# Performance work log

Hardware: AMD Instinct MI355X
Metric: run time of the kernel (lower is better)

The kernel has to match this reference:

```python
import jax, jax.numpy as jnp
import numpy as np

DMODEL, DK, DV, NHEAD = 512, 64, 64, 8
MASK_VALUE = -10000000.0


def setup_inputs() -> dict:
    key = jax.random.key(0)
    ks = jax.random.split(key, 12)
    b, slen = 8, 1024
    inputs = jax.random.normal(ks[0], (b, slen, DMODEL), dtype=jnp.float32)
    mask = (jax.random.uniform(ks[1], (b, slen, slen)) < 0.1).astype(jnp.float32)
    s = 1.0 / np.sqrt(DMODEL)
    wq = jax.random.uniform(ks[2], (DK * NHEAD, DMODEL), minval=-s, maxval=s, dtype=jnp.float32)
    bq = jnp.zeros((DK * NHEAD,), jnp.float32)
    wk = jax.random.uniform(ks[3], (DK * NHEAD, DMODEL), minval=-s, maxval=s, dtype=jnp.float32)
    bk = jnp.zeros((DK * NHEAD,), jnp.float32)
    wv = jax.random.uniform(ks[4], (DV * NHEAD, DMODEL), minval=-s, maxval=s, dtype=jnp.float32)
    bv = jnp.zeros((DV * NHEAD,), jnp.float32)
    wo = jax.random.uniform(ks[5], (DMODEL, NHEAD * DV), minval=-s, maxval=s, dtype=jnp.float32)
    bo = jnp.zeros((DMODEL,), jnp.float32)
    return {"inputs": inputs, "mask": mask, "wq": wq, "bq": bq, "wk": wk,
            "bk": bk, "wv": wv, "bv": bv, "wo": wo, "bo": bo}


def mask_logits(target, mask, mask_value=MASK_VALUE):
    return target * (1.0 - mask) + mask * mask_value


def reference(inputs, mask, wq, bq, wk, bk, wv, bv, wo, bo):
    b, slen, _ = inputs.shape
    scale = np.power(DK, 0.5).astype(np.float32)
    # projections -> [b, slen, nhead, d] -> [b, nhead, slen, d]
    q = (inputs @ wq.T + bq).reshape(b, slen, NHEAD, DK).transpose(0, 2, 1, 3)
    k = (inputs @ wk.T + bk).reshape(b, slen, NHEAD, DK).transpose(0, 2, 1, 3)
    v = (inputs @ wv.T + bv).reshape(b, slen, NHEAD, DV).transpose(0, 2, 1, 3)
    # scores [b, h, s, s]
    score = jnp.einsum("bhqd,bhkd->bhqk", q, k) / scale
    m = mask[:, None, :, :]  # broadcast over heads (original repeats mask per head)
    score = mask_logits(score, m)
    attn = jax.nn.softmax(score, axis=-1)
    attn = mask_logits(attn, m, 0.0)  # second zeroing mask pass
    # dropout is identity in eval mode
    out = jnp.einsum("bhqk,bhkd->bhqd", attn, v)  # [b, h, s, dv]
    out = out.transpose(0, 2, 1, 3).reshape(b, slen, NHEAD * DV)
    return out @ wo.T + bo
```

## Files before the change

### kernel.cpp

```cpp
#include <hip/hip_runtime.h>
#include <cstdint>
#include <cstddef>

#define NHEAD 8
#define SLEN 1024

typedef __bf16 bf16x8 __attribute__((ext_vector_type(8)));
typedef float f32x4 __attribute__((ext_vector_type(4)));

__device__ inline unsigned short f2bf(float f) {
    union { float f; unsigned int u; } v; v.f = f;
    unsigned int u = v.u;
    unsigned int rounded = u + 0x7fffu + ((u >> 16) & 1u);
    return (unsigned short)(rounded >> 16);
}

__device__ inline unsigned int pack2(float a, float b) {
    return (unsigned int)f2bf(a) | ((unsigned int)f2bf(b) << 16);
}

__device__ inline unsigned int cvtpk2(float lo, float hi) {
    unsigned int r;
    asm("v_cvt_pk_bf16_f32 %0, %1, %2" : "=v"(r) : "v"(lo), "v"(hi));
    return r;
}

__device__ inline void gll16(const unsigned short* g, unsigned short* l) {
    __builtin_amdgcn_global_load_lds(
        (const __attribute__((address_space(1))) unsigned int*)g,
        (__attribute__((address_space(3))) unsigned int*)l,
        16, 0, 0);
}

__device__ inline uint4 cvt8(const float* __restrict__ p) {
    float4 a = *reinterpret_cast<const float4*>(p);
    float4 b = *reinterpret_cast<const float4*>(p + 4);
    uint4 r;
    r.x = pack2(a.x, a.y);
    r.y = pack2(a.z, a.w);
    r.z = pack2(b.x, b.y);
    r.w = pack2(b.z, b.w);
    return r;
}

__global__ __launch_bounds__(256) void prep(
    const float* __restrict__ X,
    const float* __restrict__ wq, const float* __restrict__ wk,
    const float* __restrict__ wv, const float* __restrict__ wo,
    const float* __restrict__ mask,
    unsigned short* __restrict__ Xb, unsigned short* __restrict__ Wc,
    unsigned long long* __restrict__ bits)
{
    int y = blockIdx.y;
    if (y == 5) {
        int wid = (blockIdx.x * 256 + threadIdx.x) >> 6;
        int lane = threadIdx.x & 63;
        for (int s = 0; s < 16; s++) {
            size_t seg = (size_t)wid * 16 + s;
            float mv = mask[seg * 64 + lane];
            unsigned long long bb = __ballot(mv != 0.0f);
            if (lane == 0) bits[seg] = bb;
        }
        return;
    }
    const float* src;
    unsigned short* dst;
    int n;
    if (y == 0) { src = X;  dst = Xb; n = 8192 * 512; }
    else {
        src = (y == 1) ? wq : (y == 2) ? wk : (y == 3) ? wv : wo;
        dst = Wc + (size_t)(y - 1) * 262144;
        n = 262144;
    }
    int i = (blockIdx.x * 256 + threadIdx.x) * 8;
    if (i + 8 <= n) {
        uint4 v = cvt8(src + i);
        *reinterpret_cast<uint4*>(dst + i) = v;
    }
}

__global__ __launch_bounds__(256) void qkv_gemm(
    const unsigned short* __restrict__ Xb,
    const unsigned short* __restrict__ Wc,
    const float* __restrict__ bq, const float* __restrict__ bk,
    const float* __restrict__ bv,
    unsigned short* __restrict__ Qb, unsigned short* __restrict__ Kb,
    unsigned short* __restrict__ Vtb)
{
    __shared__ unsigned short As[128 * 136];
    unsigned short* Bs = As + 128 * 64;
    const int tid = threadIdx.x;
    const int w = tid >> 6, lane = tid & 63, l15 = lane & 15, quad = lane >> 4;
    const int wm = w & 1, wn = w >> 1;
    const int r0 = blockIdx.x * 128;
    const int ytile = blockIdx.y;
    const int c0 = ytile * 128;
    const unsigned short* Wsel = Wc + (size_t)(ytile >> 2) * 262144;
    const int cw = c0 & 511;

    f32x4 zero = {0.0f, 0.0f, 0.0f, 0.0f};
    f32x4 acc[4][4];
    for (int i = 0; i < 4; i++)
        for (int j = 0; j < 4; j++) acc[i][j] = zero;

    const int lrow = lane >> 3;
    const int lcol = (lane & 7) * 8;

    for (int k0 = 0; k0 < 512; k0 += 64) {
        const unsigned short* gA = Xb + (size_t)(r0 + w * 32 + lrow) * 512 + k0 + lcol;
        const unsigned short* gB = Wsel + (size_t)(cw + w * 32 + lrow) * 512 + k0 + lcol;
        unsigned short* lA = As + (w * 32) * 64;
        unsigned short* lB = Bs + (w * 32) * 64;
        #pragma unroll
        for (int i = 0; i < 4; i++) {
            gll16(gA + i * 8 * 512, lA + i * 8 * 64);
            gll16(gB + i * 8 * 512, lB + i * 8 * 64);
        }
        __syncthreads();
        for (int kc = 0; kc < 64; kc += 32) {
            bf16x8 af[4], bfr[4];
            for (int mi = 0; mi < 4; mi++)
                af[mi] = *reinterpret_cast<const bf16x8*>(As + (wm * 64 + mi * 16 + l15) * 64 + kc + quad * 8);
            for (int ni = 0; ni < 4; ni++)
                bfr[ni] = *reinterpret_cast<const bf16x8*>(Bs + (wn * 64 + ni * 16 + l15) * 64 + kc + quad * 8);
            for (int mi = 0; mi < 4; mi++)
                for (int ni = 0; ni < 4; ni++)
                    acc[mi][ni] = __builtin_amdgcn_mfma_f32_16x16x32_bf16(af[mi], bfr[ni], acc[mi][ni], 0, 0, 0);
        }
        __syncthreads();
    }

    const int bb = r0 >> 10;
    const int s0 = r0 & 1023;

    if (ytile < 8) {
        const bool isQ = (ytile < 4);
        const float* bias = isQ ? bq : bk;
        unsigned short* dst = isQ ? Qb : Kb;
        const float scale = isQ ? 0.125f : 1.0f;
        const int h0 = cw >> 6;
        for (int mi = 0; mi < 4; mi++) {
            for (int ni = 0; ni < 4; ni++) {
                int col = wn * 64 + ni * 16 + l15;
                float bsv = bias[cw + col];
                for (int r = 0; r < 4; r++) {
                    int s_local = wm * 64 + mi * 16 + quad * 4 + r;
                    As[s_local * 136 + col] = f2bf((acc[mi][ni][r] + bsv) * scale);
                }
            }
        }
        __syncthreads();
        for (int p = 0; p < 2; p++) {
            size_t base = (((size_t)(bb * NHEAD + h0 + p)) << 10) + s0;
            for (int i = 0; i < 4; i++) {
                int flat = i * 256 + tid;
                int row = flat >> 3;
                int ch = flat & 7;
                uint4 vv = *reinterpret_cast<const uint4*>(As + row * 136 + p * 64 + ch * 8);
                *reinterpret_cast<uint4*>(dst + (base + row) * 64 + ch * 8) = vv;
            }
        }
    } else {
        const int h_base = (c0 - 1024) >> 6;
        for (int p = 0; p < 2; p++) {
            __syncthreads();
            if (wn == p) {
                for (int mi = 0; mi < 4; mi++) {
                    for (int ni = 0; ni < 4; ni++) {
                        int d_local = ni * 16 + l15;
                        float bias = bv[(h_base + p) * 64 + d_local];
                        for (int r = 0; r < 4; r++) {
                            int s_local = wm * 64 + mi * 16 + quad * 4 + r;
                            As[d_local * 136 + s_local] = f2bf(acc[mi][ni][r] + bias);
                        }
                    }
                }
            }
            __syncthreads();
            int sidx = (tid & 15) * 8;
            int drow = tid >> 4;
            for (int dg = 0; dg < 4; dg++) {
                int d = dg * 16 + drow;
                size_t dst = ((size_t)(bb * NHEAD + h_base + p) * 64 + d) * 1024 + s0;
                uint4 vv = *reinterpret_cast<const uint4*>(As + d * 136 + sidx);
                *reinterpret_cast<uint4*>(Vtb + dst + sidx) = vv;
            }
        }
    }
}

__global__ __launch_bounds__(256, 4) void attn_kernel(
    const unsigned short* __restrict__ Qb,
    const unsigned short* __restrict__ Kb,
    const unsigned short* __restrict__ Vtb,
    const unsigned long long* __restrict__ Mbits,
    unsigned short* __restrict__ Ob)
{
    __shared__ unsigned short KVs[3 * 64 * 72];

    const int tid = threadIdx.x;
    const int w = tid >> 6, lane = tid & 63, l15 = lane & 15, quad = lane >> 4;
    const int flat = blockIdx.x;
    const int bh = flat & 63;
    const int qt = flat >> 6;
    const int b = bh >> 3, h = bh & 7;
    const int q = qt * 64 + w * 16 + l15;
    const unsigned short* Qg = Qb + (size_t)bh * SLEN * 64;
    const unsigned short* Kg = Kb + (size_t)bh * SLEN * 64;
    const unsigned short* Vg = Vtb + (size_t)bh * 64 * SLEN;
    const unsigned long long* mrow = Mbits + ((size_t)b * SLEN + q) * 16;
    unsigned short* Ks = KVs;
    unsigned short* Vs = KVs + 4608;
    unsigned short* Prow = KVs + 9216 + (size_t)(w * 16 + l15) * 72;

    bf16x8 bq0 = *reinterpret_cast<const bf16x8*>(Qg + (size_t)q * 64 + quad * 8);
    bf16x8 bq1 = *reinterpret_cast<const bf16x8*>(Qg + (size_t)q * 64 + 32 + quad * 8);

    f32x4 zero = {0.0f, 0.0f, 0.0f, 0.0f};
    f32x4 Oacc[4];
    for (int nd = 0; nd < 4; nd++) Oacc[nd] = zero;
    float lsum0 = 0.0f, lsum1 = 0.0f;

    const int srow = tid >> 3;
    const int sc8 = (tid & 7) * 8;

    uint4 kr0, kr1, vr0, vr1;
    {
        const unsigned short* kp = Kg + (size_t)srow * 64 + sc8;
        kr0 = *reinterpret_cast<const uint4*>(kp);
        kr1 = *reinterpret_cast<const uint4*>(kp + 32 * 64);
        const unsigned short* vp = Vg + (size_t)srow * SLEN + sc8;
        vr0 = *reinterpret_cast<const uint4*>(vp);
        vr1 = *reinterpret_cast<const uint4*>(vp + (size_t)32 * SLEN);
    }

    for (int kt = 0; kt < 16; kt++) {
        *reinterpret_cast<uint4*>(Ks + srow * 72 + sc8) = kr0;
        *reinterpret_cast<uint4*>(Ks + (srow + 32) * 72 + sc8) = kr1;
        *reinterpret_cast<uint4*>(Vs + srow * 72 + sc8) = vr0;
        *reinterpret_cast<uint4*>(Vs + (srow + 32) * 72 + sc8) = vr1;
        __syncthreads();

        if (kt < 15) {
            int k0n = (kt + 1) * 64;
            const unsigned short* kp = Kg + (size_t)(k0n + srow) * 64 + sc8;
            kr0 = *reinterpret_cast<const uint4*>(kp);
            kr1 = *reinterpret_cast<const uint4*>(kp + 32 * 64);
            const unsigned short* vp = Vg + (size_t)srow * SLEN + k0n + sc8;
            vr0 = *reinterpret_cast<const uint4*>(vp);
            vr1 = *reinterpret_cast<const uint4*>(vp + (size_t)32 * SLEN);
        }

        f32x4 st[4];
        for (int ni = 0; ni < 4; ni++) {
            const unsigned short* kp = Ks + (ni * 16 + l15) * 72 + quad * 8;
            bf16x8 ka0 = *reinterpret_cast<const bf16x8*>(kp);
            bf16x8 ka1 = *reinterpret_cast<const bf16x8*>(kp + 32);
            f32x4 z = zero;
            z = __builtin_amdgcn_mfma_f32_16x16x32_bf16(ka0, bq0, z, 0, 0, 0);
            z = __builtin_amdgcn_mfma_f32_16x16x32_bf16(ka1, bq1, z, 0, 0, 0);
            st[ni] = z;
        }

        unsigned long long mv = mrow[kt] >> (quad * 4);
        unsigned int lo = (unsigned int)mv, hi = (unsigned int)(mv >> 32);
        for (int ni = 0; ni < 4; ni++) {
            unsigned int word = (ni & 2) ? hi : lo;
            int sh = (ni & 1) ? 16 : 0;
            float p0 = ((word >> (sh + 0)) & 1u) ? 0.0f : __expf(st[ni][0]);
            float p1 = ((word >> (sh + 1)) & 1u) ? 0.0f : __expf(st[ni][1]);
            float p2 = ((word >> (sh + 2)) & 1u) ? 0.0f : __expf(st[ni][2]);
            float p3 = ((word >> (sh + 3)) & 1u) ? 0.0f : __expf(st[ni][3]);
            lsum0 += (p0 + p1);
            lsum1 += (p2 + p3);
            uint2 pk;
            pk.x = cvtpk2(p0, p1);
            pk.y = cvtpk2(p2, p3);
            *reinterpret_cast<uint2*>(Prow + ni * 16 + quad * 4) = pk;
        }

        bf16x8 pb0 = *reinterpret_cast<const bf16x8*>(Prow + quad * 8);
        bf16x8 pb1 = *reinterpret_cast<const bf16x8*>(Prow + 32 + quad * 8);
        for (int nd = 0; nd < 4; nd++) {
            const unsigned short* vb = Vs + (nd * 16 + l15) * 72 + quad * 8;
            bf16x8 va0 = *reinterpret_cast<const bf16x8*>(vb);
            bf16x8 va1 = *reinterpret_cast<const bf16x8*>(vb + 32);
            Oacc[nd] = __builtin_amdgcn_mfma_f32_16x16x32_bf16(va0, pb0, Oacc[nd], 0, 0, 0);
            Oacc[nd] = __builtin_amdgcn_mfma_f32_16x16x32_bf16(va1, pb1, Oacc[nd], 0, 0, 0);
        }
        __syncthreads();
    }

    float l = lsum0 + lsum1;
    l += __shfl_xor(l, 16);
    l += __shfl_xor(l, 32);
    float inv = (l > 0.0f) ? (1.0f / l) : 0.0f;
    for (int nd = 0; nd < 4; nd++) {
        uint2 o;
        o.x = cvtpk2(Oacc[nd][0] * inv, Oacc[nd][1] * inv);
        o.y = cvtpk2(Oacc[nd][2] * inv, Oacc[nd][3] * inv);
        *reinterpret_cast<uint2*>(Ob + ((size_t)(b * SLEN + q)) * 512 + h * 64 + nd * 16 + quad * 4) = o;
    }
}

__global__ __launch_bounds__(256) void out_gemm(
    const unsigned short* __restrict__ Ob,
    const unsigned short* __restrict__ Wob,
    const float* __restrict__ bo,
    float* __restrict__ out)
{
    __shared__ unsigned short As[2 * 128 * 64];
    unsigned short* Bs = As + 128 * 64;
    const int tid = threadIdx.x;
    const int w = tid >> 6, lane = tid & 63, l15 = lane & 15, quad = lane >> 4;
    const int wm = w & 1, wn = w >> 1;
    const int r0 = blockIdx.x * 128;
    const int c0 = blockIdx.y * 128;

    f32x4 zero = {0.0f, 0.0f, 0.0f, 0.0f};
    f32x4 acc[4][4];
    for (int i = 0; i < 4; i++)
        for (int j = 0; j < 4; j++) acc[i][j] = zero;

    const int lrow = lane >> 3;
    const int lcol = (lane & 7) * 8;

    for (int k0 = 0; k0 < 512; k0 += 64) {
        const unsigned short* gA = Ob + (size_t)(r0 + w * 32 + lrow) * 512 + k0 + lcol;
        const unsigned short* gB = Wob + (size_t)(c0 + w * 32 + lrow) * 512 + k0 + lcol;
        unsigned short* lA = As + (w * 32) * 64;
        unsigned short* lB = Bs + (w * 32) * 64;
        #pragma unroll
        for (int i = 0; i < 4; i++) {
            gll16(gA + i * 8 * 512, lA + i * 8 * 64);
            gll16(gB + i * 8 * 512, lB + i * 8 * 64);
        }
        __syncthreads();
        for (int kc = 0; kc < 64; kc += 32) {
            bf16x8 af[4], bfr[4];
            for (int mi = 0; mi < 4; mi++)
                af[mi] = *reinterpret_cast<const bf16x8*>(As + (wm * 64 + mi * 16 + l15) * 64 + kc + quad * 8);
            for (int ni = 0; ni < 4; ni++)
                bfr[ni] = *reinterpret_cast<const bf16x8*>(Bs + (wn * 64 + ni * 16 + l15) * 64 + kc + quad * 8);
            for (int mi = 0; mi < 4; mi++)
                for (int ni = 0; ni < 4; ni++)
                    acc[mi][ni] = __builtin_amdgcn_mfma_f32_16x16x32_bf16(af[mi], bfr[ni], acc[mi][ni], 0, 0, 0);
        }
        __syncthreads();
    }

    for (int mi = 0; mi < 4; mi++) {
        int grow_base = r0 + wm * 64 + mi * 16 + quad * 4;
        for (int ni = 0; ni < 4; ni++) {
            int gcol = c0 + wn * 64 + ni * 16 + l15;
            float bias = bo[gcol];
            for (int r = 0; r < 4; r++) {
                int grow = grow_base + r;
                out[(size_t)grow * 512 + gcol] = acc[mi][ni][r] + bias;
            }
        }
    }
}

extern "C" void kernel_launch(void* const* d_in, const int* in_sizes, int n_in,
                              void* d_out, int out_size, void* d_ws, size_t ws_size,
                              hipStream_t stream) {
    (void)in_sizes; (void)n_in; (void)out_size; (void)ws_size;
    const float* x    = (const float*)d_in[0];
    const float* mask = (const float*)d_in[1];
    const float* wq   = (const float*)d_in[2];
    const float* bq   = (const float*)d_in[3];
    const float* wk   = (const float*)d_in[4];
    const float* bk   = (const float*)d_in[5];
    const float* wv   = (const float*)d_in[6];
    const float* bv   = (const float*)d_in[7];
    const float* wo   = (const float*)d_in[8];
    const float* bo   = (const float*)d_in[9];
    float* out = (float*)d_out;

    char* ws = (char*)d_ws;
    unsigned short* Qb   = (unsigned short*)(ws);
    unsigned short* Kb   = (unsigned short*)(ws + 8388608);
    unsigned short* Vtb  = (unsigned short*)(ws + 16777216);
    unsigned short* XO   = (unsigned short*)(ws + 25165824);
    unsigned short* Wc   = (unsigned short*)(ws + 33554432);
    unsigned long long* Mbits = (unsigned long long*)(ws + 35651584);

    prep<<<dim3(2048, 6), 256, 0, stream>>>(x, wq, wk, wv, wo, mask, XO, Wc, Mbits);
    qkv_gemm<<<dim3(64, 12), 256, 0, stream>>>(XO, Wc, bq, bk, bv, Qb, Kb, Vtb);
    attn_kernel<<<dim3(1024), 256, 0, stream>>>(Qb, Kb, Vtb, Mbits, XO );
    out_gemm<<<dim3(64, 4), 256, 0, stream>>>(XO , Wc + 3 * 262144, bo, out);
}
```

Before: 198.4 us.

## Fold log2e into Q scale for raw exp2, and halve out_gemm row tile

Multiplies the Q projection scale by log2(e) so the attention kernel can use the hardware v_exp_f32 (base-2) instruction directly instead of __expf, which drops a multiply per score. Separately, the output GEMM tile shrinks from 128x128 to 64x128 rows per block, which doubles the grid to 512 blocks to improve occupancy and CU coverage on a small GEMM. The trade-off is less reuse of each weight tile and more total global loads for the weights. Dropping the max subtraction is unchanged from before, so overflow risk is the same.

```diff
diff --git a/kernel.cpp b/kernel.cpp
--- a/kernel.cpp
+++ b/kernel.cpp
@@ -25,7 +25,13 @@
     return r;
 }
 
-__device__ inline void gll16(const unsigned short* g, unsigned short* l) {
+__device__ inline float exp2i(float x) {
+    float r;
+    asm("v_exp_f32 %0, %1" : "=v"(r) : "v"(x));
+    return r;
+}
+
+__device__ inline void gll16(const void* g, void* l) {
     __builtin_amdgcn_global_load_lds(
         (const __attribute__((address_space(1))) unsigned int*)g,
         (__attribute__((address_space(3))) unsigned int*)l,
@@ -113,8 +119,8 @@
         unsigned short* lB = Bs + (w * 32) * 64;
         #pragma unroll
         for (int i = 0; i < 4; i++) {
-            gll16(gA + i * 8 * 512, lA + i * 8 * 64);
-            gll16(gB + i * 8 * 512, lB + i * 8 * 64);
+            gll16(gA + (size_t)i * 8 * 512, lA + i * 8 * 64);
+            gll16(gB + (size_t)i * 8 * 512, lB + i * 8 * 64);
         }
         __syncthreads();
         for (int kc = 0; kc < 64; kc += 32) {
@@ -137,7 +143,7 @@
         const bool isQ = (ytile < 4);
         const float* bias = isQ ? bq : bk;
         unsigned short* dst = isQ ? Qb : Kb;
-        const float scale = isQ ? 0.125f : 1.0f;
+        const float scale = isQ ? 0.18033688f : 1.0f;
         const int h0 = cw >> 6;
         for (int mi = 0; mi < 4; mi++) {
             for (int ni = 0; ni < 4; ni++) {
@@ -267,10 +273,10 @@
         for (int ni = 0; ni < 4; ni++) {
             unsigned int word = (ni & 2) ? hi : lo;
             int sh = (ni & 1) ? 16 : 0;
-            float p0 = ((word >> (sh + 0)) & 1u) ? 0.0f : __expf(st[ni][0]);
-            float p1 = ((word >> (sh + 1)) & 1u) ? 0.0f : __expf(st[ni][1]);
-            float p2 = ((word >> (sh + 2)) & 1u) ? 0.0f : __expf(st[ni][2]);
-            float p3 = ((word >> (sh + 3)) & 1u) ? 0.0f : __expf(st[ni][3]);
+            float p0 = ((word >> (sh + 0)) & 1u) ? 0.0f : exp2i(st[ni][0]);
+            float p1 = ((word >> (sh + 1)) & 1u) ? 0.0f : exp2i(st[ni][1]);
+            float p2 = ((word >> (sh + 2)) & 1u) ? 0.0f : exp2i(st[ni][2]);
+            float p3 = ((word >> (sh + 3)) & 1u) ? 0.0f : exp2i(st[ni][3]);
             lsum0 += (p0 + p1);
             lsum1 += (p2 + p3);
             uint2 pk;
@@ -309,50 +315,50 @@
     const float* __restrict__ bo,
     float* __restrict__ out)
 {
-    __shared__ unsigned short As[2 * 128 * 64];
-    unsigned short* Bs = As + 128 * 64;
+    __shared__ unsigned short As[64 * 64 + 128 * 64];
+    unsigned short* Bs = As + 64 * 64;
     const int tid = threadIdx.x;
     const int w = tid >> 6, lane = tid & 63, l15 = lane & 15, quad = lane >> 4;
-    const int wm = w & 1, wn = w >> 1;
-    const int r0 = blockIdx.x * 128;
+    const int r0 = blockIdx.x * 64;
     const int c0 = blockIdx.y * 128;
 
     f32x4 zero = {0.0f, 0.0f, 0.0f, 0.0f};
-    f32x4 acc[4][4];
+    f32x4 acc[4][2];
     for (int i = 0; i < 4; i++)
-        for (int j = 0; j < 4; j++) acc[i][j] = zero;
+        for (int j = 0; j < 2; j++) acc[i][j] = zero;
 
     const int lrow = lane >> 3;
     const int lcol = (lane & 7) * 8;
 
     for (int k0 = 0; k0 < 512; k0 += 64) {
-        const unsigned short* gA = Ob + (size_t)(r0 + w * 32 + lrow) * 512 + k0 + lcol;
+        const unsigned short* gA = Ob + (size_t)(r0 + w * 16 + lrow) * 512 + k0 + lcol;
+        unsigned short* lA = As + (w * 16) * 64;
+        #pragma unroll
+        for (int i = 0; i < 2; i++)
+            gll16(gA + (size_t)i * 8 * 512, lA + i * 8 * 64);
         const unsigned short* gB = Wob + (size_t)(c0 + w * 32 + lrow) * 512 + k0 + lcol;
-        unsigned short* lA = As + (w * 32) * 64;
         unsigned short* lB = Bs + (w * 32) * 64;
         #pragma unroll
-        for (int i = 0; i < 4; i++) {
-            gll16(gA + i * 8 * 512, lA + i * 8 * 64);
-            gll16(gB + i * 8 * 512, lB + i * 8 * 64);
-        }
+        for (int i = 0; i < 4; i++)
+            gll16(gB + (size_t)i * 8 * 512, lB + i * 8 * 64);
         __syncthreads();
         for (int kc = 0; kc < 64; kc += 32) {
-            bf16x8 af[4], bfr[4];
+            bf16x8 af[4], bfr[2];
             for (int mi = 0; mi < 4; mi++)
-                af[mi] = *reinterpret_cast<const bf16x8*>(As + (wm * 64 + mi * 16 + l15) * 64 + kc + quad * 8);
-            for (int ni = 0; ni < 4; ni++)
-                bfr[ni] = *reinterpret_cast<const bf16x8*>(Bs + (wn * 64 + ni * 16 + l15) * 64 + kc + quad * 8);
+                af[mi] = *reinterpret_cast<const bf16x8*>(As + (mi * 16 + l15) * 64 + kc + quad * 8);
+            for (int ni = 0; ni < 2; ni++)
+                bfr[ni] = *reinterpret_cast<const bf16x8*>(Bs + (w * 32 + ni * 16 + l15) * 64 + kc + quad * 8);
             for (int mi = 0; mi < 4; mi++)
-                for (int ni = 0; ni < 4; ni++)
+                for (int ni = 0; ni < 2; ni++)
                     acc[mi][ni] = __builtin_amdgcn_mfma_f32_16x16x32_bf16(af[mi], bfr[ni], acc[mi][ni], 0, 0, 0);
         }
         __syncthreads();
     }
 
     for (int mi = 0; mi < 4; mi++) {
-        int grow_base = r0 + wm * 64 + mi * 16 + quad * 4;
-        for (int ni = 0; ni < 4; ni++) {
-            int gcol = c0 + wn * 64 + ni * 16 + l15;
+        int grow_base = r0 + mi * 16 + quad * 4;
+        for (int ni = 0; ni < 2; ni++) {
+            int gcol = c0 + w * 32 + ni * 16 + l15;
             float bias = bo[gcol];
             for (int r = 0; r < 4; r++) {
                 int grow = grow_base + r;
@@ -389,5 +395,5 @@
     prep<<<dim3(2048, 6), 256, 0, stream>>>(x, wq, wk, wv, wo, mask, XO, Wc, Mbits);
     qkv_gemm<<<dim3(64, 12), 256, 0, stream>>>(XO, Wc, bq, bk, bv, Qb, Kb, Vtb);
     attn_kernel<<<dim3(1024), 256, 0, stream>>>(Qb, Kb, Vtb, Mbits, XO );
-    out_gemm<<<dim3(64, 4), 256, 0, stream>>>(XO , Wc + 3 * 262144, bo, out);
-}
+    out_gemm<<<dim3(128, 4), 256, 0, stream>>>(XO , Wc + 3 * 262144, bo, out);
+}
```

Result: no change. 195.9 us (-1.2%).
